# Kernel tuning notes

Hardware: AMD Instinct MI355X
Metric: run time of the kernel (lower is better)

The kernel has to match this reference:

```python
import jax, jax.numpy as jnp
import numpy as np

NUM_HEADS = 16


def setup_inputs() -> dict:
    key = jax.random.key(0)
    ks = jax.random.split(key, 5)
    B, N, D = 2, 2048, 1024
    scale = 1.0 / np.sqrt(D)  # roughly xavier-ish magnitude for weights
    return {
        "x": jax.random.normal(ks[0], (B, N, D), dtype=jnp.float32),
        "W_query": jax.random.normal(ks[1], (D, D), dtype=jnp.float32) * scale,
        "W_key": jax.random.normal(ks[2], (D, D), dtype=jnp.float32) * scale,
        "W_value": jax.random.normal(ks[3], (D, D), dtype=jnp.float32) * scale,
        "W_output": jax.random.normal(ks[4], (D, D), dtype=jnp.float32) * scale,
    }


def reference(x, W_query, W_key, W_value, W_output):
    # x: [B, N, D]; weights: [D, D]
    B, N, D = x.shape
    H = NUM_HEADS
    hd = D // H

    def mh_embed(W):
        # linear_embedding then split heads: [B, N, D] -> [B, H, N, hd]
        y = jnp.einsum("bnd,de->bne", x, W)
        return y.reshape(B, N, H, hd).transpose(0, 2, 1, 3)

    q = mh_embed(W_query)
    k = mh_embed(W_key)
    v = mh_embed(W_value)

    # NOTE: source scales by token_dim**-0.5 (full model dim), not head_dim
    attn = jnp.einsum("bhnd,bhmd->bhnm", q, k) * (D ** -0.5)
    attn = jax.nn.softmax(attn, axis=-1)
    out = jnp.einsum("bhnm,bhmd->bhnd", attn, v)  # [B, H, N, hd]

    out = out.transpose(0, 2, 1, 3).reshape(B, N, D)  # merge heads
    out = jnp.einsum("bnd,de->bne", out, W_output)
    return out
```

## Files before the change

kernel.cpp:

```cpp
#include <hip/hip_runtime.h>

#define D_MODEL 1024
#define N_TOK   2048
#define NHEAD   16
#define HDIM    64
#define BATCH   2
#define M_TOT   (BATCH*N_TOK)

typedef unsigned short u16;
typedef __bf16 bf16x8 __attribute__((ext_vector_type(8)));
typedef float  f32x4  __attribute__((ext_vector_type(4)));

#define QSCALE 0.04508422002777439f

__device__ __forceinline__ u16 f2bf(float f) {
  union { float f; unsigned u; } v; v.f = f;
  unsigned r = v.u + 0x7fffu + ((v.u >> 16) & 1u);
  return (u16)(r >> 16);
}

__device__ __forceinline__ float bf2f(u16 u) {
  union { unsigned u; float f; } v; v.u = ((unsigned)u) << 16; return v.f;
}

__device__ __forceinline__ unsigned pk2bf(float a, float b) {
#if __has_builtin(__builtin_amdgcn_cvt_pk_bf16_f32)
  typedef __bf16 bf16x2_t __attribute__((ext_vector_type(2)));
  bf16x2_t r = __builtin_amdgcn_cvt_pk_bf16_f32(a, b);
  union { bf16x2_t v; unsigned u; } c; c.v = r; return c.u;
#else
  return (unsigned)f2bf(a) | ((unsigned)f2bf(b) << 16);
#endif
}

__device__ __forceinline__ void gl2lds16(const void* g, void* l) {
  __builtin_amdgcn_global_load_lds(
      (__attribute__((address_space(1))) void*)g,
      (__attribute__((address_space(3))) void*)l, 16, 0, 0);
}

__global__ void prep_kernel(const float* __restrict__ x,
                            const float* __restrict__ s0, const float* __restrict__ s1,
                            const float* __restrict__ s2, const float* __restrict__ s3,
                            u16* __restrict__ xb,
                            u16* __restrict__ d0, u16* __restrict__ d1,
                            u16* __restrict__ d2, u16* __restrict__ d3) {
  const int t = threadIdx.y * 32 + threadIdx.x;
  if (blockIdx.z == 4) {
    int base = (blockIdx.y * 32 + blockIdx.x) * 256 + t;
#pragma unroll
    for (int r = 0; r < 4; ++r) {
      int i = base + r * 262144;
      float4 v = ((const float4*)x)[i];
      ushort4 o;
      o.x = f2bf(v.x); o.y = f2bf(v.y); o.z = f2bf(v.z); o.w = f2bf(v.w);
      ((ushort4*)xb)[i] = o;
    }
    return;
  }
  const float* src; u16* dst;
  switch (blockIdx.z) {
    case 0:  src = s0; dst = d0; break;
    case 1:  src = s1; dst = d1; break;
    case 2:  src = s2; dst = d2; break;
    default: src = s3; dst = d3; break;
  }
  float sc = (blockIdx.z == 0) ? QSCALE : 1.0f;
  __shared__ float tile[32][33];
  int xg = blockIdx.x * 32 + threadIdx.x;
  int ybase = blockIdx.y * 32;
#pragma unroll
  for (int r = 0; r < 4; ++r)
    tile[threadIdx.y + r*8][threadIdx.x] = src[(size_t)(ybase + threadIdx.y + r*8)*D_MODEL + xg];
  __syncthreads();
#pragma unroll
  for (int r = 0; r < 4; ++r)
    dst[(size_t)(blockIdx.x*32 + threadIdx.y + r*8)*D_MODEL + ybase + threadIdx.x] =
        f2bf(tile[threadIdx.x][threadIdx.y + r*8] * sc);
}

__device__ __forceinline__ void gemm_body(const u16* __restrict__ A,
                                          const u16* __restrict__ Bt,
                                          void* __restrict__ Cout, int mode) {
  __shared__ __attribute__((aligned(16))) u16 lA[2][128*32];
  __shared__ __attribute__((aligned(16))) u16 lB[2][128*32];
  const int t = threadIdx.x;
  const int lane = t & 63, w = t >> 6;
  const int wm = w >> 1, wn = w & 1;
  const int q4 = lane >> 4, l15 = lane & 15;
  const int m0 = blockIdx.y * 128, n0 = blockIdx.x * 128;

  const int c0 = t, c1 = 256 + t;
  const int r0 = c0 >> 2, g0 = (c0 & 3) ^ (r0 & 3);
  const int r1 = c1 >> 2, g1 = (c1 & 3) ^ (r1 & 3);

  f32x4 acc[4][4] = {};

  gl2lds16(A  + (size_t)(m0 + r0)*D_MODEL + g0*8, &lA[0][c0*8]);
  gl2lds16(Bt + (size_t)(n0 + r0)*D_MODEL + g0*8, &lB[0][c0*8]);
  gl2lds16(A  + (size_t)(m0 + r1)*D_MODEL + g1*8, &lA[0][c1*8]);
  gl2lds16(Bt + (size_t)(n0 + r1)*D_MODEL + g1*8, &lB[0][c1*8]);

  for (int it = 0; it < 32; ++it) {
    const int cur = it & 1;
    __syncthreads();
    if (it + 1 < 32) {
      const int kn = (it + 1) * 32;
      u16* dA = &lA[cur ^ 1][0]; u16* dB = &lB[cur ^ 1][0];
      gl2lds16(A  + (size_t)(m0 + r0)*D_MODEL + kn + g0*8, dA + c0*8);
      gl2lds16(Bt + (size_t)(n0 + r0)*D_MODEL + kn + g0*8, dB + c0*8);
      gl2lds16(A  + (size_t)(m0 + r1)*D_MODEL + kn + g1*8, dA + c1*8);
      gl2lds16(Bt + (size_t)(n0 + r1)*D_MODEL + kn + g1*8, dB + c1*8);
    }
    const u16* sA = &lA[cur][0]; const u16* sB = &lB[cur][0];
    bf16x8 af[4], bfr[4];
#pragma unroll
    for (int mi = 0; mi < 4; ++mi) {
      int r = wm*64 + mi*16 + l15;
      af[mi] = *(const bf16x8*)(sA + r*32 + ((q4 ^ (r & 3)) * 8));
    }
#pragma unroll
    for (int ni = 0; ni < 4; ++ni) {
      int r = wn*64 + ni*16 + l15;
      bfr[ni] = *(const bf16x8*)(sB + r*32 + ((q4 ^ (r & 3)) * 8));
    }
#pragma unroll
    for (int mi = 0; mi < 4; ++mi)
#pragma unroll
      for (int ni = 0; ni < 4; ++ni)
        acc[mi][ni] = __builtin_amdgcn_mfma_f32_16x16x32_bf16(af[mi], bfr[ni], acc[mi][ni], 0, 0, 0);
  }

#pragma unroll
  for (int mi = 0; mi < 4; ++mi) {
#pragma unroll
    for (int ni = 0; ni < 4; ++ni) {
      const int tok0 = m0 + wm*64 + mi*16 + q4*4;
      const int col  = n0 + wn*64 + ni*16 + l15;
      if (mode == 0) {
        u16* D = (u16*)Cout;
#pragma unroll
        for (int r = 0; r < 4; ++r) {
          int tok = tok0 + r;
          int b = tok >> 11, n = tok & (N_TOK-1);
          int h = col >> 6, d = col & (HDIM-1);
          D[(((size_t)(b*NHEAD + h))*N_TOK + n)*HDIM + d] = f2bf(acc[mi][ni][r]);
        }
      } else {
        int b = tok0 >> 11, n = tok0 & (N_TOK-1);
        int h = col >> 6, d = col & (HDIM-1);
        ushort4 pk;
        pk.x = f2bf(acc[mi][ni][0]); pk.y = f2bf(acc[mi][ni][1]);
        pk.z = f2bf(acc[mi][ni][2]); pk.w = f2bf(acc[mi][ni][3]);
        *(ushort4*)((u16*)Cout + ((size_t)(b*NHEAD + h)*HDIM + d)*N_TOK + n) = pk;
      }
    }
  }
}

__global__ __launch_bounds__(256) void qkv_kernel(const u16* __restrict__ xb,
    const u16* __restrict__ wqt, const u16* __restrict__ wkt, const u16* __restrict__ wvt,
    u16* __restrict__ Q, u16* __restrict__ K, u16* __restrict__ Vt) {
  int z = blockIdx.z;
  const u16* B = (z == 0) ? wqt : (z == 1) ? wkt : wvt;
  void* C = (z == 0) ? (void*)Q : (z == 1) ? (void*)K : (void*)Vt;
  gemm_body(xb, B, C, (z == 2) ? 2 : 0);
}

__global__ __launch_bounds__(256) void out_kernel(const u16* __restrict__ ctx,
    const u16* __restrict__ wot, float* __restrict__ out) {
  __shared__ __attribute__((aligned(16))) u16 lA[2][64*32];
  __shared__ __attribute__((aligned(16))) u16 lB[2][128*32];
  const int t = threadIdx.x;
  const int lane = t & 63, w = t >> 6;
  const int wm = w >> 1, wn = w & 1;
  const int q4 = lane >> 4, l15 = lane & 15;
  const int m0 = blockIdx.y * 64, n0 = blockIdx.x * 128;

  const int rA = t >> 2, gA = (t & 3) ^ (rA & 3);
  const int c0 = t, c1 = 256 + t;
  const int r0 = c0 >> 2, g0 = (c0 & 3) ^ (r0 & 3);
  const int r1 = c1 >> 2, g1 = (c1 & 3) ^ (r1 & 3);

  f32x4 acc[2][4] = {};

  gl2lds16(ctx + (size_t)(m0 + rA)*D_MODEL + gA*8, &lA[0][t*8]);
  gl2lds16(wot + (size_t)(n0 + r0)*D_MODEL + g0*8, &lB[0][c0*8]);
  gl2lds16(wot + (size_t)(n0 + r1)*D_MODEL + g1*8, &lB[0][c1*8]);

  for (int it = 0; it < 32; ++it) {
    const int cur = it & 1;
    __syncthreads();
    if (it + 1 < 32) {
      const int kn = (it + 1) * 32;
      u16* dA = &lA[cur ^ 1][0]; u16* dB = &lB[cur ^ 1][0];
      gl2lds16(ctx + (size_t)(m0 + rA)*D_MODEL + kn + gA*8, dA + t*8);
      gl2lds16(wot + (size_t)(n0 + r0)*D_MODEL + kn + g0*8, dB + c0*8);
      gl2lds16(wot + (size_t)(n0 + r1)*D_MODEL + kn + g1*8, dB + c1*8);
    }
    const u16* sA = &lA[cur][0]; const u16* sB = &lB[cur][0];
    bf16x8 af[2], bfr[4];
#pragma unroll
    for (int mi = 0; mi < 2; ++mi) {
      int r = wm*32 + mi*16 + l15;
      af[mi] = *(const bf16x8*)(sA + r*32 + ((q4 ^ (r & 3)) * 8));
    }
#pragma unroll
    for (int ni = 0; ni < 4; ++ni) {
      int r = wn*64 + ni*16 + l15;
      bfr[ni] = *(const bf16x8*)(sB + r*32 + ((q4 ^ (r & 3)) * 8));
    }
#pragma unroll
    for (int mi = 0; mi < 2; ++mi)
#pragma unroll
      for (int ni = 0; ni < 4; ++ni)
        acc[mi][ni] = __builtin_amdgcn_mfma_f32_16x16x32_bf16(af[mi], bfr[ni], acc[mi][ni], 0, 0, 0);
  }

#pragma unroll
  for (int mi = 0; mi < 2; ++mi) {
#pragma unroll
    for (int ni = 0; ni < 4; ++ni) {
      const int tok0 = m0 + wm*32 + mi*16 + q4*4;
      const int col  = n0 + wn*64 + ni*16 + l15;
#pragma unroll
      for (int r = 0; r < 4; ++r)
        out[(size_t)(tok0 + r)*D_MODEL + col] = acc[mi][ni][r];
    }
  }
}

__global__ __launch_bounds__(256, 3) void attn_kernel(const u16* __restrict__ Qg,
    const u16* __restrict__ Kg, const u16* __restrict__ Vtg,
    u16* __restrict__ Opart, float* __restrict__ Lpart) {
  __shared__ __attribute__((aligned(16))) u16 lds[24576];
  const int t = threadIdx.x;
  const int lane = t & 63, w = t >> 6;
  const int q4 = lane >> 4, l15 = lane & 15;
  const int bh = blockIdx.y;
  const int qb = blockIdx.x >> 1, half = blockIdx.x & 1;
  const int qw0 = qb * 128 + w * 32;
  const size_t kvBase = (size_t)bh * (N_TOK * HDIM);
  u16* myP = lds + 16384 + w * 2048;

  const int ck0 = t, ck1 = 256 + t;
  const int kr0 = ck0 >> 3, kg0 = (ck0 & 7) ^ (kr0 & 7);
  const int kr1 = ck1 >> 3, kg1 = (ck1 & 7) ^ (kr1 & 7);

  bf16x8 qf[2][2];
#pragma unroll
  for (int ni = 0; ni < 2; ++ni)
#pragma unroll
    for (int kk = 0; kk < 2; ++kk)
      qf[ni][kk] = *(const bf16x8*)(Qg + kvBase +
                    (size_t)(qw0 + ni*16 + l15)*HDIM + kk*32 + q4*8);

  f32x4 accO[4][2] = {};
  float lsum[2] = {0.f, 0.f};

  const int kvStart = half * 1024;
  gl2lds16(Kg  + kvBase + (size_t)(kvStart + kr0)*HDIM + kg0*8, lds + ck0*8);
  gl2lds16(Kg  + kvBase + (size_t)(kvStart + kr1)*HDIM + kg1*8, lds + ck1*8);
  gl2lds16(Vtg + kvBase + (size_t)kr0*N_TOK + kvStart + kg0*8,  lds + 8192 + ck0*8);
  gl2lds16(Vtg + kvBase + (size_t)kr1*N_TOK + kvStart + kg1*8,  lds + 8192 + ck1*8);

  for (int it = 0; it < 16; ++it) {
    const int cur = it & 1;
    __syncthreads();
    if (it + 1 < 16) {
      const int kvn = kvStart + (it + 1) * 64;
      u16* dK = lds + (cur ^ 1) * 4096;
      u16* dV = lds + 8192 + (cur ^ 1) * 4096;
      gl2lds16(Kg  + kvBase + (size_t)(kvn + kr0)*HDIM + kg0*8, dK + ck0*8);
      gl2lds16(Kg  + kvBase + (size_t)(kvn + kr1)*HDIM + kg1*8, dK + ck1*8);
      gl2lds16(Vtg + kvBase + (size_t)kr0*N_TOK + kvn + kg0*8,  dV + ck0*8);
      gl2lds16(Vtg + kvBase + (size_t)kr1*N_TOK + kvn + kg1*8,  dV + ck1*8);
    }
    const u16* sK = lds + cur * 4096;
    const u16* sV = lds + 8192 + cur * 4096;

#pragma unroll
    for (int mip = 0; mip < 4; ++mip) {
      const int kv = mip*16 + l15;
      f32x4 s[2] = {};
#pragma unroll
      for (int kk = 0; kk < 2; ++kk) {
        bf16x8 a = *(const bf16x8*)(sK + kv*64 + (((kk*4 + q4) ^ (l15 & 7)) * 8));
#pragma unroll
        for (int ni = 0; ni < 2; ++ni)
          s[ni] = __builtin_amdgcn_mfma_f32_16x16x32_bf16(a, qf[ni][kk], s[ni], 0, 0, 0);
      }
#pragma unroll
      for (int ni = 0; ni < 2; ++ni) {
        float p0 = __builtin_amdgcn_exp2f(s[ni][0]);
        float p1 = __builtin_amdgcn_exp2f(s[ni][1]);
        float p2 = __builtin_amdgcn_exp2f(s[ni][2]);
        float p3 = __builtin_amdgcn_exp2f(s[ni][3]);
        lsum[ni] += (p0 + p1) + (p2 + p3);
        uint2 u; u.x = pk2bf(p0, p1); u.y = pk2bf(p2, p3);
        const int qloc = ni*16 + l15;
        const int kv8 = mip*4 + q4;
        *(uint2*)(myP + qloc*64 + (((kv8 >> 1) ^ (qloc & 7)) * 8) + (kv8 & 1)*4) = u;
      }
    }

#pragma unroll
    for (int kk2 = 0; kk2 < 2; ++kk2) {
      bf16x8 bp[2];
#pragma unroll
      for (int ni = 0; ni < 2; ++ni)
        bp[ni] = *(const bf16x8*)(myP + (ni*16 + l15)*64 +
                                  (((kk2*4 + q4) ^ (l15 & 7)) * 8));
#pragma unroll
      for (int mi2 = 0; mi2 < 4; ++mi2) {
        const int d = mi2*16 + l15;
        bf16x8 av = *(const bf16x8*)(sV + d*64 + (((kk2*4 + q4) ^ (d & 7)) * 8));
#pragma unroll
        for (int ni = 0; ni < 2; ++ni)
          accO[mi2][ni] = __builtin_amdgcn_mfma_f32_16x16x32_bf16(av, bp[ni], accO[mi2][ni], 0, 0, 0);
      }
    }
  }

  const int b = bh >> 4, head = bh & (NHEAD-1);
  u16* Obase = Opart + (size_t)half * (M_TOT * D_MODEL);
#pragma unroll
  for (int ni = 0; ni < 2; ++ni) {
    float ls = lsum[ni];
    ls += __shfl_xor(ls, 16);
    ls += __shfl_xor(ls, 32);
    const int q = qw0 + ni*16 + l15;
    if (q4 == 0)
      Lpart[(size_t)half*(32*N_TOK) + bh*N_TOK + q] = ls;
    const size_t rb = ((size_t)(b*N_TOK + q))*D_MODEL + head*HDIM + q4*4;
#pragma unroll
    for (int mi2 = 0; mi2 < 4; ++mi2) {
      uint2 u;
      u.x = pk2bf(accO[mi2][ni][0], accO[mi2][ni][1]);
      u.y = pk2bf(accO[mi2][ni][2], accO[mi2][ni][3]);
      *(uint2*)(Obase + rb + mi2*16) = u;
    }
  }
}

__global__ __launch_bounds__(256) void combine_kernel(const u16* __restrict__ Opart,
    const float* __restrict__ Lpart, u16* __restrict__ ctx) {
  int i = blockIdx.x * 256 + threadIdx.x;
  int tok = i >> 7, c8 = i & 127;
  int n = tok & (N_TOK-1), b = tok >> 11;
  int h = c8 >> 3;
  int bh = b*NHEAD + h;
  float l = Lpart[(size_t)bh*N_TOK + n] + Lpart[(size_t)(32*N_TOK) + bh*N_TOK + n];
  float inv = 1.0f / l;
  const size_t off = (size_t)tok*D_MODEL + c8*8;
  ushort4 a0 = *(const ushort4*)(Opart + off);
  ushort4 a1 = *(const ushort4*)(Opart + off + 4);
  ushort4 b0 = *(const ushort4*)(Opart + (size_t)(M_TOT*D_MODEL) + off);
  ushort4 b1 = *(const ushort4*)(Opart + (size_t)(M_TOT*D_MODEL) + off + 4);
  uint2 o0, o1;
  o0.x = pk2bf((bf2f(a0.x)+bf2f(b0.x))*inv, (bf2f(a0.y)+bf2f(b0.y))*inv);
  o0.y = pk2bf((bf2f(a0.z)+bf2f(b0.z))*inv, (bf2f(a0.w)+bf2f(b0.w))*inv);
  o1.x = pk2bf((bf2f(a1.x)+bf2f(b1.x))*inv, (bf2f(a1.y)+bf2f(b1.y))*inv);
  o1.y = pk2bf((bf2f(a1.z)+bf2f(b1.z))*inv, (bf2f(a1.w)+bf2f(b1.w))*inv);
  *(uint2*)(ctx + off) = o0;
  *(uint2*)(ctx + off + 4) = o1;
}

extern "C" void kernel_launch(void* const* d_in, const int* in_sizes, int n_in,
                              void* d_out, int out_size, void* d_ws, size_t ws_size,
                              hipStream_t stream) {
  const float* x  = (const float*)d_in[0];
  const float* Wq = (const float*)d_in[1];
  const float* Wk = (const float*)d_in[2];
  const float* Wv = (const float*)d_in[3];
  const float* Wo = (const float*)d_in[4];
  float* out = (float*)d_out;

  char* ws = (char*)d_ws;
  u16* xb   = (u16*)(ws);
  u16* wqt  = (u16*)(ws + (8u  << 20));
  u16* wkt  = (u16*)(ws + (10u << 20));
  u16* wvt  = (u16*)(ws + (12u << 20));
  u16* wot  = (u16*)(ws + (14u << 20));
  u16* Qw   = (u16*)(ws + (16u << 20));
  u16* Kw   = (u16*)(ws + (24u << 20));
  u16* Vtw  = (u16*)(ws + (32u << 20));
  u16* ctx  = (u16*)(ws + (40u << 20));
  u16* Op   = (u16*)(ws + (48u << 20));
  float* Lp = (float*)(ws + (64u << 20));
  (void)in_sizes; (void)n_in; (void)out_size; (void)ws_size;

  prep_kernel<<<dim3(32, 32, 5), dim3(32, 8), 0, stream>>>(x, Wq, Wk, Wv, Wo,
                                                           xb, wqt, wkt, wvt, wot);
  qkv_kernel<<<dim3(8, 32, 3), 256, 0, stream>>>(xb, wqt, wkt, wvt, Qw, Kw, Vtw);
  attn_kernel<<<dim3(32, 32), 256, 0, stream>>>(Qw, Kw, Vtw, Op, Lp);
  combine_kernel<<<2048, 256, 0, stream>>>(Op, Lp, ctx);
  out_kernel<<<dim3(8, 64), 256, 0, stream>>>(ctx, wot, out);
}
```

Measured before the change: 202.0 us.

## Keep softmax probabilities in registers via permlane16 swap instead of LDS round-trip

Stops writing the P tile to shared memory and reading it back. The bf16 probabilities stay in registers, and v_permlane16_swap builds the MFMA B operand directly. The V read index is permuted to match the new k ordering. Dropping the P buffer shrinks LDS, which allows 4 blocks per CU instead of 3, and s_setprio hints are added around the MFMA sections. The risks are higher register pressure under the tighter occupancy bound and correctness depending on the lane permutation matching.

New measurement: 205.7 us. About the same (+1.8%).

```diff
diff --git a/kernel.cpp b/kernel.cpp
--- a/kernel.cpp
+++ b/kernel.cpp
@@ -230,18 +230,18 @@
   }
 }
 
-__global__ __launch_bounds__(256, 3) void attn_kernel(const u16* __restrict__ Qg,
+__global__ __launch_bounds__(256, 4) void attn_kernel(const u16* __restrict__ Qg,
     const u16* __restrict__ Kg, const u16* __restrict__ Vtg,
     u16* __restrict__ Opart, float* __restrict__ Lpart) {
-  __shared__ __attribute__((aligned(16))) u16 lds[24576];
+  __shared__ __attribute__((aligned(16))) u16 lds[16384];
   const int t = threadIdx.x;
   const int lane = t & 63, w = t >> 6;
   const int q4 = lane >> 4, l15 = lane & 15;
+  const int q4sw = ((q4 & 1) << 1) | (q4 >> 1);
   const int bh = blockIdx.y;
   const int qb = blockIdx.x >> 1, half = blockIdx.x & 1;
   const int qw0 = qb * 128 + w * 32;
   const size_t kvBase = (size_t)bh * (N_TOK * HDIM);
-  u16* myP = lds + 16384 + w * 2048;
 
   const int ck0 = t, ck1 = 256 + t;
   const int kr0 = ck0 >> 3, kg0 = (ck0 & 7) ^ (kr0 & 7);
@@ -279,10 +279,12 @@
     const u16* sK = lds + cur * 4096;
     const u16* sV = lds + 8192 + cur * 4096;
 
+    unsigned wv[4][2][2];
 #pragma unroll
     for (int mip = 0; mip < 4; ++mip) {
       const int kv = mip*16 + l15;
       f32x4 s[2] = {};
+      __builtin_amdgcn_s_setprio(1);
 #pragma unroll
       for (int kk = 0; kk < 2; ++kk) {
         bf16x8 a = *(const bf16x8*)(sK + kv*64 + (((kk*4 + q4) ^ (l15 & 7)) * 8));
@@ -290,6 +292,7 @@
         for (int ni = 0; ni < 2; ++ni)
           s[ni] = __builtin_amdgcn_mfma_f32_16x16x32_bf16(a, qf[ni][kk], s[ni], 0, 0, 0);
       }
+      __builtin_amdgcn_s_setprio(0);
 #pragma unroll
       for (int ni = 0; ni < 2; ++ni) {
         float p0 = __builtin_amdgcn_exp2f(s[ni][0]);
@@ -297,29 +300,38 @@
         float p2 = __builtin_amdgcn_exp2f(s[ni][2]);
         float p3 = __builtin_amdgcn_exp2f(s[ni][3]);
         lsum[ni] += (p0 + p1) + (p2 + p3);
-        uint2 u; u.x = pk2bf(p0, p1); u.y = pk2bf(p2, p3);
-        const int qloc = ni*16 + l15;
-        const int kv8 = mip*4 + q4;
-        *(uint2*)(myP + qloc*64 + (((kv8 >> 1) ^ (qloc & 7)) * 8) + (kv8 & 1)*4) = u;
+        wv[mip][ni][0] = pk2bf(p0, p1);
+        wv[mip][ni][1] = pk2bf(p2, p3);
       }
     }
 
+    bf16x8 bp[2][2];
+#pragma unroll
+    for (int ni = 0; ni < 2; ++ni)
+#pragma unroll
+      for (int kk2 = 0; kk2 < 2; ++kk2) {
+        unsigned x0 = wv[2*kk2][ni][0], x1 = wv[2*kk2][ni][1];
+        unsigned y0 = wv[2*kk2+1][ni][0], y1 = wv[2*kk2+1][ni][1];
+        asm("v_permlane16_swap_b32 %0, %1" : "+v"(x0), "+v"(y0));
+        asm("v_permlane16_swap_b32 %0, %1" : "+v"(x1), "+v"(y1));
+        union { unsigned u[4]; bf16x8 v; } pb;
+        pb.u[0] = x0; pb.u[1] = x1; pb.u[2] = y0; pb.u[3] = y1;
+        bp[ni][kk2] = pb.v;
+      }
+
+    __builtin_amdgcn_s_setprio(1);
 #pragma unroll
     for (int kk2 = 0; kk2 < 2; ++kk2) {
-      bf16x8 bp[2];
-#pragma unroll
-      for (int ni = 0; ni < 2; ++ni)
-        bp[ni] = *(const bf16x8*)(myP + (ni*16 + l15)*64 +
-                                  (((kk2*4 + q4) ^ (l15 & 7)) * 8));
 #pragma unroll
       for (int mi2 = 0; mi2 < 4; ++mi2) {
         const int d = mi2*16 + l15;
-        bf16x8 av = *(const bf16x8*)(sV + d*64 + (((kk2*4 + q4) ^ (d & 7)) * 8));
+        bf16x8 av = *(const bf16x8*)(sV + d*64 + (((kk2*4 + q4sw) ^ (d & 7)) * 8));
 #pragma unroll
         for (int ni = 0; ni < 2; ++ni)
-          accO[mi2][ni] = __builtin_amdgcn_mfma_f32_16x16x32_bf16(av, bp[ni], accO[mi2][ni], 0, 0, 0);
+          accO[mi2][ni] = __builtin_amdgcn_mfma_f32_16x16x32_bf16(av, bp[ni][kk2], accO[mi2][ni], 0, 0, 0);
       }
     }
+    __builtin_amdgcn_s_setprio(0);
   }
 
   const int b = bh >> 4, head = bh & (NHEAD-1);
```
